# Kernel tuning notes

Hardware: AMD Instinct MI355X
Metric: run time of the kernel (lower is better)

## Reference

```python
import jax, jax.numpy as jnp
import numpy as np

B, T, N, E = 4, 8, 3000, 12000
D = 256; H = 256; HEADS = 8; DH = H // HEADS; F = 8; L = 3; HD = 64
NEG_SLOPE = 0.2


def layer_norm(x, g, b):
    m = x.mean(-1, keepdims=True)
    v = x.var(-1, keepdims=True)
    return (x - m) / jnp.sqrt(v + 1e-5) * g + b


def gat(x, edge_emb, src, dst, W, We, a_src, a_dst, a_edge):
    # x: [B,N,Din], edge_emb: [B,E,H] -> [B,N,H] via edge-conditioned graph attention
    Bc, Nc = x.shape[0], x.shape[1]
    xw = (x @ W).reshape(Bc, Nc, HEADS, DH)
    ew = (edge_emb @ We).reshape(Bc, -1, HEADS, DH)
    xs = xw[:, src]  # [B,E,HEADS,DH] gather
    xd = xw[:, dst]
    logit = (xs * a_src).sum(-1) + (xd * a_dst).sum(-1) + (ew * a_edge).sum(-1)  # [B,E,HEADS]
    logit = jnp.where(logit > 0, logit, NEG_SLOPE * logit)  # leaky_relu(0.2)

    def seg_softmax(lg):  # softmax over incoming edges per dst node
        m = jax.ops.segment_max(lg, dst, num_segments=Nc)
        e = jnp.exp(lg - m[dst])
        s = jax.ops.segment_sum(e, dst, num_segments=Nc)
        return e / (s[dst] + 1e-16)

    w = jax.vmap(seg_softmax)(logit)  # [B,E,HEADS]
    msg = (xs + ew) * w[..., None]
    out = jax.vmap(lambda m_: jax.ops.segment_sum(m_, dst, num_segments=Nc))(msg)
    return out.reshape(Bc, Nc, H)


def mlp(x, w1, b1, w2, b2):
    return jax.nn.relu(x @ w1 + b1) @ w2 + b2


def setup_inputs() -> dict:
    key = jax.random.key(0)
    ks = iter(jax.random.split(key, 64))
    rn = lambda s, sc=1.0: jax.random.normal(next(ks), s, dtype=jnp.float32) * sc
    return {
        'env_emb': rn((B, T, N, D)), 'infra_emb': rn((B, T, N, D)), 'robot_emb': rn((B, T, N, D)),
        'edge_attr': rn((B, E, F)),
        'edge_index': jax.random.randint(next(ks), (2, E), 0, N),
        'wqkv': rn((D, 3 * D), 0.05), 'bqkv': jnp.zeros((3 * D,), jnp.float32),
        'wo': rn((D, D), 0.05), 'bo': jnp.zeros((D,), jnp.float32),
        'lnf_g': jnp.ones((D,), jnp.float32), 'lnf_b': jnp.zeros((D,), jnp.float32),
        'we_emb': rn((F, H), 0.1), 'be_emb': jnp.zeros((H,), jnp.float32),
        'tg_W': rn((D, H), 0.05), 'tg_We': rn((H, H), 0.05),
        'tg_asrc': rn((HEADS, DH), 0.1), 'tg_adst': rn((HEADS, DH), 0.1), 'tg_aedge': rn((HEADS, DH), 0.1),
        'w_ih': rn((H, 4 * H), 0.05), 'w_hh': rn((H, 4 * H), 0.05), 'b_lstm': jnp.zeros((4 * H,), jnp.float32),
        'g_W': rn((L, H, H), 0.05), 'g_We': rn((L, H, H), 0.05),
        'g_asrc': rn((L, HEADS, DH), 0.1), 'g_adst': rn((L, HEADS, DH), 0.1), 'g_aedge': rn((L, HEADS, DH), 0.1),
        'g_lng': jnp.ones((L, H), jnp.float32), 'g_lnb': jnp.zeros((L, H), jnp.float32),
        'hn_w1': rn((8, H, HD), 0.05), 'hn_b1': jnp.zeros((8, HD), jnp.float32),
        'hn_w2': rn((8, HD, 1), 0.05), 'hn_b2': jnp.zeros((8, 1), jnp.float32),
        'he_w1': rn((2, 2 * H, HD), 0.05), 'he_b1': jnp.zeros((2, HD), jnp.float32),
        'he_w2': rn((2, HD, 1), 0.05), 'he_b2': jnp.zeros((2, 1), jnp.float32),
    }


def reference(env_emb, infra_emb, robot_emb, edge_attr, edge_index,
              wqkv, bqkv, wo, bo, lnf_g, lnf_b, we_emb, be_emb,
              tg_W, tg_We, tg_asrc, tg_adst, tg_aedge,
              w_ih, w_hh, b_lstm,
              g_W, g_We, g_asrc, g_adst, g_aedge, g_lng, g_lnb,
              hn_w1, hn_b1, hn_w2, hn_b2, he_w1, he_b1, he_w2, he_b2):
    # --- per-timestep 3-token cross-modal self-attention, vectorized over B,T,N ---
    tokens = jnp.stack([env_emb, infra_emb, robot_emb], axis=3)  # [B,T,N,3,D]
    qkv = tokens @ wqkv + bqkv
    q, k, v = jnp.split(qkv, 3, axis=-1)
    sh = tokens.shape[:-1] + (HEADS, DH)
    q = q.reshape(sh); k = k.reshape(sh); v = v.reshape(sh)
    att = jax.nn.softmax(jnp.einsum('btnqhd,btnkhd->btnhqk', q, k) / np.sqrt(DH).astype(np.float32), axis=-1)
    o = jnp.einsum('btnhqk,btnkhd->btnqhd', att, v).reshape(tokens.shape)
    fused_seq = layer_norm((o @ wo + bo).mean(axis=3), lnf_g, lnf_b)  # [B,T,N,D]

    edge_emb = jax.nn.relu(edge_attr @ we_emb + be_emb)  # [B,E,H]
    src = edge_index[0]; dst = edge_index[1]

    # --- TemporalGNNCell: GAT message passing feeding an LSTM cell, scanned over T ---
    def step(carry, x_t):
        h, c = carry
        m = gat(x_t, edge_emb, src, dst, tg_W, tg_We, tg_asrc, tg_adst, tg_aedge)
        gates = m @ w_ih + h @ w_hh + b_lstm
        i, f, g, oo = jnp.split(gates, 4, axis=-1)
        c = jax.nn.sigmoid(f) * c + jax.nn.sigmoid(i) * jnp.tanh(g)
        h = jax.nn.sigmoid(oo) * jnp.tanh(c)
        return (h, c), None

    z = jnp.zeros((B, N, H), fused_seq.dtype)
    (h, _), _ = jax.lax.scan(step, (z, z), jnp.moveaxis(fused_seq, 1, 0))

    # --- stacked residual GAT layers with LayerNorm ---
    for i in range(L):
        h_new = gat(h, edge_emb, src, dst, g_W[i], g_We[i], g_asrc[i], g_adst[i], g_aedge[i])
        h = layer_norm(h + h_new, g_lng[i], g_lnb[i])

    # --- prediction heads ---
    failure = jax.nn.sigmoid(mlp(h, hn_w1[0], hn_b1[0], hn_w2[0], hn_b2[0]))
    timing = jax.nn.softplus(mlp(h, hn_w1[1], hn_b1[1], hn_w2[1], hn_b2[1]))
    others = [mlp(h, hn_w1[j], hn_b1[j], hn_w2[j], hn_b2[j]) for j in range(2, 6)]  # voltage, angle, temperature, reactive
    risk = jax.nn.sigmoid(mlp(h, hn_w1[6], hn_b1[6], hn_w2[6], hn_b2[6]))
    node_out = jnp.concatenate([failure, timing] + others + [risk], axis=-1)  # [B,N,7]
    h_global = h.mean(axis=1, keepdims=True)
    freq = mlp(h_global, hn_w1[7], hn_b1[7], hn_w2[7], hn_b2[7]).reshape(B, 1)
    ef = jnp.concatenate([h[:, src], h[:, dst]], axis=-1)  # [B,E,2H]
    line = mlp(ef, he_w1[0], he_b1[0], he_w2[0], he_b2[0])
    active = mlp(ef, he_w1[1], he_b1[1], he_w2[1], he_b2[1])
    return jnp.concatenate([node_out.reshape(B, -1), line.reshape(B, -1), active.reshape(B, -1), freq], axis=1)
```

## Files before the change

kernel.cpp:

```cpp
#include <hip/hip_runtime.h>
#include <hip/hip_bf16.h>
#include <math.h>

#define DEV __device__ __forceinline__

namespace {
constexpr int B_ = 4, T_ = 8, N_ = 3000, E_ = 12000;
constexpr int OUTS_ = 45001;
}

using f32x4 = __attribute__((ext_vector_type(4))) float;
using bf16x8 = __attribute__((ext_vector_type(8))) short;

DEV float sigm_(float x) { return 1.0f / (1.0f + expf(-x)); }
DEV float softplus_(float x) { return fmaxf(x, 0.0f) + log1pf(expf(-fabsf(x))); }
DEV float wred_(float v) {
  #pragma unroll
  for (int o = 32; o > 0; o >>= 1) v += __shfl_xor(v, o, 64);
  return v;
}
DEV unsigned short f2bf(float x) {
  unsigned u = __float_as_uint(x);
  return (unsigned short)((u + 0x7FFFu + ((u >> 16) & 1u)) >> 16);
}
DEV unsigned f2bf2(float a, float b) {
  return (unsigned)f2bf(a) | ((unsigned)f2bf(b) << 16);
}
DEV float bfl(unsigned u) { return __uint_as_float(u << 16); }
DEV float bfh(unsigned u) { return __uint_as_float(u & 0xffff0000u); }

__global__ void wtb_k(const float* __restrict__ W, unsigned short* __restrict__ Wt,
                      int K, int N, int total)
{
  const int idx = blockIdx.x * blockDim.x + threadIdx.x;
  if (idx >= total) return;
  const int kn = K * N;
  const int l = idx / kn;
  const int r = idx - l * kn;
  const int k = r / N, n = r - k * N;
  Wt[(size_t)l * kn + (size_t)n * K + k] = f2bf(W[idx]);
}

__global__ void wtp_k(const float* __restrict__ W, unsigned short* __restrict__ Wt,
                      int kOff)
{
  const int idx = blockIdx.x * blockDim.x + threadIdx.x;
  if (idx >= 256 * 1024) return;
  const int k = idx >> 10;
  const int n = idx & 1023;
  const int newcol = (n & 255) * 4 + (n >> 8);
  Wt[(size_t)newcol * 512 + kOff + k] = f2bf(W[idx]);
}

__global__ void hist_k(const int* __restrict__ dst, int* __restrict__ deg)
{
  const int e = blockIdx.x * blockDim.x + threadIdx.x;
  if (e < E_) atomicAdd(&deg[dst[e]], 1);
}

__global__ __launch_bounds__(256) void scan_k(const int* __restrict__ deg,
                                              int* __restrict__ roff)
{
  __shared__ int part[256];
  const int t = threadIdx.x;
  int loc[12];
  int s = 0;
  #pragma unroll
  for (int i = 0; i < 12; ++i) {
    const int n = t * 12 + i;
    loc[i] = s;
    s += (n < N_) ? deg[n] : 0;
  }
  part[t] = s;
  __syncthreads();
  if (t == 0) {
    int run = 0;
    for (int i = 0; i < 256; ++i) { const int v = part[i]; part[i] = run; run += v; }
  }
  __syncthreads();
  const int base = part[t];
  #pragma unroll
  for (int i = 0; i < 12; ++i) {
    const int n = t * 12 + i;
    if (n < N_) roff[n] = base + loc[i];
  }
  if (t == 0) roff[N_] = E_;
}

__global__ __launch_bounds__(256) void fill_k(const int* __restrict__ dst,
                                              const int* __restrict__ roff,
                                              int* __restrict__ eord)
{
  const int n = blockIdx.x * 4 + (threadIdx.x >> 6);
  if (n >= N_) return;
  const int lane = threadIdx.x & 63;
  const unsigned long long ltm = (1ull << lane) - 1ull;
  int cnt = roff[n];
  for (int c = 0; c < E_; c += 64) {
    const int e = c + lane;
    const bool m = (e < E_) && (dst[e] == n);
    const unsigned long long mask = __ballot(m);
    if (m) eord[cnt + __popcll(mask & ltm)] = e;
    cnt += __popcll(mask);
  }
}

__global__ __launch_bounds__(256) void gemm_bfa_k(
    const unsigned short* __restrict__ A, const unsigned short* __restrict__ Wt,
    const float* __restrict__ bias, void* __restrict__ Cv,
    int M, int N, int K, int lda, int flags)
{
  __shared__ unsigned short Al[128 * 40];
  __shared__ unsigned short Bl[64 * 40];
  const int tid = threadIdx.x;
  const int bm = blockIdx.y * 128;
  const int bn = blockIdx.x * 64;
  const int lane = tid & 63;
  const int wv = tid >> 6;
  const int wm = (wv >> 1) * 64;
  const int wn = (wv & 1) * 32;
  const int s_row = tid >> 1;
  const int s_cb = (tid & 1) * 16;
  const int grow = bm + s_row;
  const unsigned short* Arow = (grow < M) ? A + (size_t)grow * lda : nullptr;
  const int b_col = tid >> 2;
  const int b_ks = (tid & 3) * 8;
  const unsigned short* Wrow = Wt + (size_t)(bn + b_col) * K + b_ks;

  f32x4 acc[4][2] = {};
  const int l15 = lane & 15;
  const int lk = (lane >> 4) * 8;

  for (int k0 = 0; k0 < K; k0 += 32) {
    uint4 a0, a1;
    if (Arow) {
      a0 = *(const uint4*)(Arow + k0 + s_cb);
      a1 = *(const uint4*)(Arow + k0 + s_cb + 8);
    } else {
      a0 = make_uint4(0, 0, 0, 0);
      a1 = a0;
    }
    *(uint4*)&Al[s_row * 40 + s_cb] = a0;
    *(uint4*)&Al[s_row * 40 + s_cb + 8] = a1;
    *(uint4*)&Bl[b_col * 40 + b_ks] = *(const uint4*)(Wrow + k0);
    __syncthreads();
    bf16x8 af[4], bfr[2];
    #pragma unroll
    for (int m = 0; m < 4; ++m)
      af[m] = *(const bf16x8*)&Al[(wm + m * 16 + l15) * 40 + lk];
    #pragma unroll
    for (int n = 0; n < 2; ++n)
      bfr[n] = *(const bf16x8*)&Bl[(wn + n * 16 + l15) * 40 + lk];
    #pragma unroll
    for (int m = 0; m < 4; ++m)
      #pragma unroll
      for (int n = 0; n < 2; ++n)
        acc[m][n] = __builtin_amdgcn_mfma_f32_16x16x32_bf16(af[m], bfr[n], acc[m][n], 0, 0, 0);
    __syncthreads();
  }
  float* Cf = (float*)Cv;
  unsigned short* Cb = (unsigned short*)Cv;
  const int r4 = (lane >> 4) * 4;
  #pragma unroll
  for (int m = 0; m < 4; ++m) {
    #pragma unroll
    for (int n = 0; n < 2; ++n) {
      const int col = bn + wn + n * 16 + l15;
      const float bv = bias ? bias[col] : 0.f;
      #pragma unroll
      for (int r = 0; r < 4; ++r) {
        const int row = bm + wm + m * 16 + r4 + r;
        if (row >= M) continue;
        float v = acc[m][n][r] + bv;
        const size_t ci = (size_t)row * N + col;
        if (flags & 1) v += Cf[ci];
        if (flags & 2) v = fmaxf(v, 0.f);
        if (flags & 4) Cb[ci] = f2bf(v);
        else Cf[ci] = v;
      }
    }
  }
}

__global__ __launch_bounds__(256) void gemm_qkv_k(
    const float* __restrict__ env, const float* __restrict__ infra,
    const float* __restrict__ robot, const unsigned short* __restrict__ Wt,
    const float* __restrict__ bias, unsigned short* __restrict__ Cb,
    int M, int nodeBase)
{
  __shared__ unsigned short Al[128 * 40];
  __shared__ unsigned short Bl[64 * 40];
  const int tid = threadIdx.x;
  const int bm = blockIdx.y * 128;
  const int bn = blockIdx.x * 64;
  const int lane = tid & 63;
  const int wv = tid >> 6;
  const int wm = (wv >> 1) * 64;
  const int wn = (wv & 1) * 32;
  const int s_row = tid >> 1;
  const int s_cb = (tid & 1) * 16;
  const int grow = bm + s_row;
  const float* Arow = nullptr;
  if (grow < M) {
    const int slot = grow % 3;
    const int node = nodeBase + grow / 3;
    const float* srcp = (slot == 0 ? env : (slot == 1 ? infra : robot));
    Arow = srcp + (size_t)node * 256;
  }
  const int b_col = tid >> 2;
  const int b_ks = (tid & 3) * 8;
  const unsigned short* Wrow = Wt + (size_t)(bn + b_col) * 256 + b_ks;

  f32x4 acc[4][2] = {};
  const int l15 = lane & 15;
  const int lk = (lane >> 4) * 8;

  for (int k0 = 0; k0 < 256; k0 += 32) {
    unsigned abuf[8];
    if (Arow) {
      const float* p = Arow + k0 + s_cb;
      #pragma unroll
      for (int i = 0; i < 4; ++i) {
        const float4 v = *(const float4*)(p + i * 4);
        abuf[i * 2 + 0] = f2bf2(v.x, v.y);
        abuf[i * 2 + 1] = f2bf2(v.z, v.w);
      }
    } else {
      #pragma unroll
      for (int i = 0; i < 8; ++i) abuf[i] = 0;
    }
    *(uint4*)&Al[s_row * 40 + s_cb] = *(uint4*)&abuf[0];
    *(uint4*)&Al[s_row * 40 + s_cb + 8] = *(uint4*)&abuf[4];
    *(uint4*)&Bl[b_col * 40 + b_ks] = *(const uint4*)(Wrow + k0);
    __syncthreads();
    bf16x8 af[4], bfr[2];
    #pragma unroll
    for (int m = 0; m < 4; ++m)
      af[m] = *(const bf16x8*)&Al[(wm + m * 16 + l15) * 40 + lk];
    #pragma unroll
    for (int n = 0; n < 2; ++n)
      bfr[n] = *(const bf16x8*)&Bl[(wn + n * 16 + l15) * 40 + lk];
    #pragma unroll
    for (int m = 0; m < 4; ++m)
      #pragma unroll
      for (int n = 0; n < 2; ++n)
        acc[m][n] = __builtin_amdgcn_mfma_f32_16x16x32_bf16(af[m], bfr[n], acc[m][n], 0, 0, 0);
    __syncthreads();
  }
  const int r4 = (lane >> 4) * 4;
  #pragma unroll
  for (int m = 0; m < 4; ++m) {
    #pragma unroll
    for (int n = 0; n < 2; ++n) {
      const int col = bn + wn + n * 16 + l15;
      const float bv = bias[col];
      #pragma unroll
      for (int r = 0; r < 4; ++r) {
        const int row = bm + wm + m * 16 + r4 + r;
        if (row >= M) continue;
        Cb[(size_t)row * 768 + col] = f2bf(acc[m][n][r] + bv);
      }
    }
  }
}

__global__ __launch_bounds__(256) void gemm_lstm_k(
    const unsigned short* __restrict__ gatall, const unsigned short* __restrict__ hbIn,
    const unsigned short* __restrict__ Wt, const float* __restrict__ b_lstm,
    float* __restrict__ h, float* __restrict__ c, unsigned short* __restrict__ hbOut,
    int t)
{
  __shared__ float Gl[128][65];
  unsigned short* Al = (unsigned short*)&Gl[0][0];
  unsigned short* Bl = Al + 128 * 40;
  const int tid = threadIdx.x;
  const int bm = blockIdx.y * 128;
  const int bn = blockIdx.x * 64;
  const int lane = tid & 63;
  const int wv = tid >> 6;
  const int wm = (wv >> 1) * 64;
  const int wn = (wv & 1) * 32;
  const int s_row = tid >> 1;
  const int s_cb = (tid & 1) * 16;
  const int grow = bm + s_row;
  const unsigned short* Arow1 = nullptr;
  const unsigned short* Arow2 = nullptr;
  if (grow < 12000) {
    const int phys = (grow / N_) * (T_ * N_) + t * N_ + (grow % N_);
    Arow1 = gatall + (size_t)phys * 256;
    Arow2 = hbIn + (size_t)grow * 256;
  }
  const int b_col = tid >> 2;
  const int b_ks = (tid & 3) * 8;
  const unsigned short* Wrow = Wt + (size_t)(bn + b_col) * 512 + b_ks;

  f32x4 acc[4][2] = {};
  const int l15 = lane & 15;
  const int lk = (lane >> 4) * 8;

  for (int k0 = 0; k0 < 512; k0 += 32) {
    uint4 a0, a1;
    if (Arow1) {
      const unsigned short* p = (k0 < 256) ? (Arow1 + k0 + s_cb)
                                           : (Arow2 + (k0 - 256) + s_cb);
      a0 = *(const uint4*)p;
      a1 = *(const uint4*)(p + 8);
    } else {
      a0 = make_uint4(0, 0, 0, 0);
      a1 = a0;
    }
    *(uint4*)&Al[s_row * 40 + s_cb] = a0;
    *(uint4*)&Al[s_row * 40 + s_cb + 8] = a1;
    *(uint4*)&Bl[b_col * 40 + b_ks] = *(const uint4*)(Wrow + k0);
    __syncthreads();
    bf16x8 af[4], bfr[2];
    #pragma unroll
    for (int m = 0; m < 4; ++m)
      af[m] = *(const bf16x8*)&Al[(wm + m * 16 + l15) * 40 + lk];
    #pragma unroll
    for (int n = 0; n < 2; ++n)
      bfr[n] = *(const bf16x8*)&Bl[(wn + n * 16 + l15) * 40 + lk];
    #pragma unroll
    for (int m = 0; m < 4; ++m)
      #pragma unroll
      for (int n = 0; n < 2; ++n)
        acc[m][n] = __builtin_amdgcn_mfma_f32_16x16x32_bf16(af[m], bfr[n], acc[m][n], 0, 0, 0);
    __syncthreads();
  }
  const int r4 = (lane >> 4) * 4;
  #pragma unroll
  for (int m = 0; m < 4; ++m)
    #pragma unroll
    for (int n = 0; n < 2; ++n) {
      const int col = wn + n * 16 + l15;
      #pragma unroll
      for (int r = 0; r < 4; ++r)
        Gl[wm + m * 16 + r4 + r][col] = acc[m][n][r];
    }
  __syncthreads();
  const int fl = lane & 7;
  const int rg = lane >> 3;
  const int dg = ((bn + wn) >> 2) + fl;
  const float bi = b_lstm[dg];
  const float bff = b_lstm[256 + dg];
  const float bg = b_lstm[512 + dg];
  const float bo = b_lstm[768 + dg];
  const int colb = wn + fl * 4;
  #pragma unroll
  for (int i = 0; i < 8; ++i) {
    const int rl = rg + i * 8;
    const int row = bm + wm + rl;
    if (row >= 12000) continue;
    const float g0 = Gl[wm + rl][colb + 0] + bi;
    const float g1 = Gl[wm + rl][colb + 1] + bff;
    const float g2 = Gl[wm + rl][colb + 2] + bg;
    const float g3 = Gl[wm + rl][colb + 3] + bo;
    const size_t idx = (size_t)row * 256 + dg;
    const float cn = sigm_(g1) * c[idx] + sigm_(g0) * tanhf(g2);
    c[idx] = cn;
    const float hn = sigm_(g3) * tanhf(cn);
    h[idx] = hn;
    hbOut[idx] = f2bf(hn);
  }
}

__global__ __launch_bounds__(256) void gemm_k(
    const float* __restrict__ A, const float* __restrict__ W,
    const float* __restrict__ bias, void* __restrict__ Cv,
    int M, int N, int K, int lda, int flags)
{
  __shared__ float As[16][68];
  __shared__ float Ws[16][64];
  const int tid = threadIdx.x;
  const int bm = blockIdx.y * 64;
  const int bn = blockIdx.x * 64;
  const int tx = tid & 15;
  const int ty = tid >> 4;
  const int ar = tid >> 2;
  const int ac = (tid & 3) << 2;
  const int wr = tid >> 4;
  const int wc = (tid & 15) << 2;
  const int grow = bm + ar;
  const float* Arow = (grow < M) ? A + (size_t)grow * lda : nullptr;
  float acc[4][4] = {};
  for (int k0 = 0; k0 < K; k0 += 16) {
    float4 av = make_float4(0.f, 0.f, 0.f, 0.f);
    if (Arow) {
      av.x = (k0 + ac + 0 < K) ? Arow[k0 + ac + 0] : 0.f;
      av.y = (k0 + ac + 1 < K) ? Arow[k0 + ac + 1] : 0.f;
      av.z = (k0 + ac + 2 < K) ? Arow[k0 + ac + 2] : 0.f;
      av.w = (k0 + ac + 3 < K) ? Arow[k0 + ac + 3] : 0.f;
    }
    As[ac + 0][ar] = av.x;
    As[ac + 1][ar] = av.y;
    As[ac + 2][ar] = av.z;
    As[ac + 3][ar] = av.w;
    float4 wv = make_float4(0.f, 0.f, 0.f, 0.f);
    if (k0 + wr < K) {
      const int gc = bn + wc;
      const float* wp = W + (size_t)(k0 + wr) * N + gc;
      wv.x = (gc + 0 < N) ? wp[0] : 0.f;
      wv.y = (gc + 1 < N) ? wp[1] : 0.f;
      wv.z = (gc + 2 < N) ? wp[2] : 0.f;
      wv.w = (gc + 3 < N) ? wp[3] : 0.f;
    }
    *(float4*)&Ws[wr][wc] = wv;
    __syncthreads();
    #pragma unroll
    for (int kk = 0; kk < 16; ++kk) {
      const float4 a = *(const float4*)&As[kk][ty << 2];
      const float4 b = *(const float4*)&Ws[kk][tx << 2];
      acc[0][0] += a.x * b.x; acc[0][1] += a.x * b.y; acc[0][2] += a.x * b.z; acc[0][3] += a.x * b.w;
      acc[1][0] += a.y * b.x; acc[1][1] += a.y * b.y; acc[1][2] += a.y * b.z; acc[1][3] += a.y * b.w;
      acc[2][0] += a.z * b.x; acc[2][1] += a.z * b.y; acc[2][2] += a.z * b.z; acc[2][3] += a.z * b.w;
      acc[3][0] += a.w * b.x; acc[3][1] += a.w * b.y; acc[3][2] += a.w * b.z; acc[3][3] += a.w * b.w;
    }
    __syncthreads();
  }
  float* Cf = (float*)Cv;
  unsigned short* Cb = (unsigned short*)Cv;
  #pragma unroll
  for (int i = 0; i < 4; ++i) {
    const int row = bm + (ty << 2) + i;
    if (row >= M) continue;
    #pragma unroll
    for (int j = 0; j < 4; ++j) {
      const int col = bn + (tx << 2) + j;
      if (col >= N) continue;
      float v = acc[i][j];
      if (bias) v += bias[col];
      if (flags & 2) v = fmaxf(v, 0.f);
      const size_t ci = (size_t)row * N + col;
      if (flags & 4) Cb[ci] = f2bf(v);
      else Cf[ci] = v;
    }
  }
}

__global__ __launch_bounds__(256) void attn_avg_k(
    const unsigned short* __restrict__ qkv,
    unsigned short* __restrict__ obar, int nodes)
{
  const int node = blockIdx.x * 4 + (threadIdx.x >> 6);
  if (node >= nodes) return;
  const int lane = threadIdx.x & 63;
  const unsigned short* base = qkv + (size_t)node * 2304 + lane * 4;
  float qv[3][4], kv[3][4], vv[3][4];
  #pragma unroll
  for (int s = 0; s < 3; ++s) {
    const uint2 uq = *(const uint2*)(base + s * 768);
    const uint2 uk = *(const uint2*)(base + s * 768 + 256);
    const uint2 uv = *(const uint2*)(base + s * 768 + 512);
    qv[s][0] = bfl(uq.x); qv[s][1] = bfh(uq.x); qv[s][2] = bfl(uq.y); qv[s][3] = bfh(uq.y);
    kv[s][0] = bfl(uk.x); kv[s][1] = bfh(uk.x); kv[s][2] = bfl(uk.y); kv[s][3] = bfh(uk.y);
    vv[s][0] = bfl(uv.x); vv[s][1] = bfh(uv.x); vv[s][2] = bfl(uv.y); vv[s][3] = bfh(uv.y);
  }
  float att[3][3];
  #pragma unroll
  for (int s = 0; s < 3; ++s) {
    #pragma unroll
    for (int t = 0; t < 3; ++t) {
      float d = qv[s][0] * kv[t][0] + qv[s][1] * kv[t][1]
              + qv[s][2] * kv[t][2] + qv[s][3] * kv[t][3];
      d += __shfl_xor(d, 1, 64);
      d += __shfl_xor(d, 2, 64);
      d += __shfl_xor(d, 4, 64);
      att[s][t] = d * 0.17677669529663687f;
    }
  }
  float cs[3] = {0.f, 0.f, 0.f};
  #pragma unroll
  for (int s = 0; s < 3; ++s) {
    const float m = fmaxf(att[s][0], fmaxf(att[s][1], att[s][2]));
    const float e0 = expf(att[s][0] - m);
    const float e1 = expf(att[s][1] - m);
    const float e2 = expf(att[s][2] - m);
    const float inv = (1.f / 3.f) / (e0 + e1 + e2);
    cs[0] += e0 * inv; cs[1] += e1 * inv; cs[2] += e2 * inv;
  }
  float o0 = cs[0] * vv[0][0] + cs[1] * vv[1][0] + cs[2] * vv[2][0];
  float o1 = cs[0] * vv[0][1] + cs[1] * vv[1][1] + cs[2] * vv[2][1];
  float o2 = cs[0] * vv[0][2] + cs[1] * vv[1][2] + cs[2] * vv[2][2];
  float o3 = cs[0] * vv[0][3] + cs[1] * vv[1][3] + cs[2] * vv[2][3];
  uint2 ob;
  ob.x = f2bf2(o0, o1);
  ob.y = f2bf2(o2, o3);
  *(uint2*)(obar + (size_t)node * 256 + lane * 4) = ob;
}

__global__ __launch_bounds__(64) void ln_k(
    const float* __restrict__ in, const float* __restrict__ g,
    const float* __restrict__ bta, unsigned short* __restrict__ outp)
{
  const int row = blockIdx.x;
  const int d0 = threadIdx.x << 2;
  const float4 a = *(const float4*)(in + (size_t)row * 256 + d0);
  float x[4] = { a.x, a.y, a.z, a.w };
  float s = x[0] + x[1] + x[2] + x[3];
  s = wred_(s);
  const float mean = s * (1.f / 256.f);
  float vs = 0.f;
  #pragma unroll
  for (int i = 0; i < 4; ++i) { const float dd = x[i] - mean; vs += dd * dd; }
  vs = wred_(vs);
  const float inv = 1.0f / sqrtf(vs * (1.f / 256.f) + 1e-5f);
  const float4 gv = *(const float4*)(g + d0);
  const float4 bv = *(const float4*)(bta + d0);
  uint2 o;
  o.x = f2bf2((x[0] - mean) * inv * gv.x + bv.x, (x[1] - mean) * inv * gv.y + bv.y);
  o.y = f2bf2((x[2] - mean) * inv * gv.z + bv.z, (x[3] - mean) * inv * gv.w + bv.w);
  *(uint2*)(outp + (size_t)row * 256 + d0) = o;
}

__global__ void alphas_k(const unsigned short* __restrict__ xw, const float* __restrict__ as,
                         const float* __restrict__ ad, float* __restrict__ sal,
                         float* __restrict__ dal, int rows)
{
  const int idx = blockIdx.x * blockDim.x + threadIdx.x;
  if (idx >= rows * 8) return;
  const int row = idx >> 3, h = idx & 7;
  const unsigned short* x = xw + (size_t)row * 256 + h * 32;
  const float* a1 = as + h * 32;
  const float* a2 = ad + h * 32;
  float s = 0.f, d = 0.f;
  #pragma unroll
  for (int i = 0; i < 4; ++i) {
    const uint4 ux = *(const uint4*)(x + i * 8);
    const unsigned* p = &ux.x;
    #pragma unroll
    for (int j = 0; j < 4; ++j) {
      const float lo = bfl(p[j]), hi = bfh(p[j]);
      s += lo * a1[i * 8 + 2 * j] + hi * a1[i * 8 + 2 * j + 1];
      d += lo * a2[i * 8 + 2 * j] + hi * a2[i * 8 + 2 * j + 1];
    }
  }
  sal[idx] = s; dal[idx] = d;
}

__global__ void elog4_k(const unsigned short* __restrict__ ew,
                        const float* __restrict__ tg_ae, const float* __restrict__ g_ae,
                        float* __restrict__ el)
{
  const int idx = blockIdx.x * blockDim.x + threadIdx.x;
  if (idx >= 4 * 48000 * 8) return;
  const int l = idx / (48000 * 8);
  const int r = idx - l * (48000 * 8);
  const int row = r >> 3, h = r & 7;
  const unsigned short* x = ew + (size_t)row * 1024 + l * 256 + h * 32;
  const float* a1 = (l == 0 ? tg_ae : g_ae + (l - 1) * 256) + h * 32;
  float s = 0.f;
  #pragma unroll
  for (int i = 0; i < 4; ++i) {
    const uint4 ux = *(const uint4*)(x + i * 8);
    const unsigned* p = &ux.x;
    #pragma unroll
    for (int j = 0; j < 4; ++j) {
      s += bfl(p[j]) * a1[i * 8 + 2 * j] + bfh(p[j]) * a1[i * 8 + 2 * j + 1];
    }
  }
  el[l * 384000 + r] = s;
}

template<int OUTBF>
__global__ __launch_bounds__(256) void gat_k(
    const unsigned short* __restrict__ xw, const unsigned short* __restrict__ ew,
    const float* __restrict__ sal, const float* __restrict__ dal,
    const float* __restrict__ el, const int* __restrict__ roff,
    const int* __restrict__ eord, const int* __restrict__ srcArr,
    void* __restrict__ outp, int nwaves, int tshift, int ewStride, int ewOff)
{
  const int wid = blockIdx.x * 4 + (threadIdx.x >> 6);
  if (wid >= nwaves) return;
  const int beta = wid / N_;
  const int n = wid - beta * N_;
  const int b = beta >> tshift;
  const int lane = threadIdx.x & 63;
  const int h = lane >> 3;
  const int d0 = lane << 2;
  const float dal_h = dal[(size_t)wid * 8 + h];
  const int p0 = roff[n], p1 = roff[n + 1];
  float m = -1e30f, s = 0.f;
  float4 acc = make_float4(0.f, 0.f, 0.f, 0.f);
  for (int p = p0; p < p1; ++p) {
    const int e = eord[p];
    const int sc = srcArr[e];
    float lg = sal[((size_t)beta * N_ + sc) * 8 + h] + dal_h + el[((size_t)b * E_ + e) * 8 + h];
    lg = lg > 0.f ? lg : 0.2f * lg;
    const float mn = fmaxf(m, lg);
    const float scale = expf(m - mn);
    const float w = expf(lg - mn);
    s = s * scale + w;
    const uint2 ux = *(const uint2*)(xw + ((size_t)beta * N_ + sc) * 256 + d0);
    const uint2 ue = *(const uint2*)(ew + ((size_t)(b * E_ + e)) * ewStride + ewOff + d0);
    acc.x = acc.x * scale + w * (bfl(ux.x) + bfl(ue.x));
    acc.y = acc.y * scale + w * (bfh(ux.x) + bfh(ue.x));
    acc.z = acc.z * scale + w * (bfl(ux.y) + bfl(ue.y));
    acc.w = acc.w * scale + w * (bfh(ux.y) + bfh(ue.y));
    m = mn;
  }
  const float inv = 1.0f / (s + 1e-16f);
  if (OUTBF) {
    uint2 o;
    o.x = f2bf2(acc.x * inv, acc.y * inv);
    o.y = f2bf2(acc.z * inv, acc.w * inv);
    *(uint2*)((unsigned short*)outp + (size_t)wid * 256 + d0) = o;
  } else {
    *(float4*)((float*)outp + (size_t)wid * 256 + d0) =
        make_float4(acc.x * inv, acc.y * inv, acc.z * inv, acc.w * inv);
  }
}

__global__ __launch_bounds__(64) void resln_k(float* __restrict__ h,
                                              const float* __restrict__ add,
                                              const float* __restrict__ g,
                                              const float* __restrict__ bta,
                                              unsigned short* __restrict__ hb)
{
  const int row = blockIdx.x;
  const int d0 = threadIdx.x << 2;
  float* hp = h + (size_t)row * 256;
  const float4 hv = *(const float4*)(hp + d0);
  const float4 av = *(const float4*)(add + (size_t)row * 256 + d0);
  float x[4] = { hv.x + av.x, hv.y + av.y, hv.z + av.z, hv.w + av.w };
  float s = x[0] + x[1] + x[2] + x[3];
  s = wred_(s);
  const float mean = s * (1.f / 256.f);
  float vs = 0.f;
  #pragma unroll
  for (int i = 0; i < 4; ++i) { const float dd = x[i] - mean; vs += dd * dd; }
  vs = wred_(vs);
  const float inv = 1.0f / sqrtf(vs * (1.f / 256.f) + 1e-5f);
  const float4 gv = *(const float4*)(g + d0);
  const float4 bv = *(const float4*)(bta + d0);
  float o0 = (x[0] - mean) * inv * gv.x + bv.x;
  float o1 = (x[1] - mean) * inv * gv.y + bv.y;
  float o2 = (x[2] - mean) * inv * gv.z + bv.z;
  float o3 = (x[3] - mean) * inv * gv.w + bv.w;
  *(float4*)(hp + d0) = make_float4(o0, o1, o2, o3);
  uint2 ob;
  ob.x = f2bf2(o0, o1);
  ob.y = f2bf2(o2, o3);
  *(uint2*)(hb + (size_t)row * 256 + d0) = ob;
}

__global__ void nh2_k(const float* __restrict__ hidden, const float* __restrict__ w2,
                      const float* __restrict__ b2, float* __restrict__ outp)
{
  const int idx = blockIdx.x * blockDim.x + threadIdx.x;
  if (idx >= B_ * N_ * 7) return;
  const int row = idx / 7, j = idx % 7;
  const float* hp = hidden + (size_t)row * 448 + j * 64;
  const float* wp = w2 + j * 64;
  float a = 0.f;
  #pragma unroll
  for (int u = 0; u < 64; ++u) a += hp[u] * wp[u];
  a += b2[j];
  if (j == 0 || j == 6) a = sigm_(a);
  else if (j == 1) a = softplus_(a);
  const int b = row / N_, n = row % N_;
  outp[(size_t)b * OUTS_ + n * 7 + j] = a;
}

__global__ __launch_bounds__(256) void hglob1_k(const float* __restrict__ h,
                                                float* __restrict__ hgp)
{
  const int b = blockIdx.x;
  const int seg = blockIdx.y;
  const int d = threadIdx.x;
  float s = 0.f;
  const int n0 = seg * 120;
  for (int n = n0; n < n0 + 120; ++n)
    s += h[((size_t)(b * N_ + n)) * 256 + d];
  hgp[((size_t)(b * 25 + seg)) * 256 + d] = s;
}

__global__ __launch_bounds__(256) void hglob2_k(const float* __restrict__ hgp,
                                                float* __restrict__ hg)
{
  const int b = blockIdx.x;
  const int d = threadIdx.x;
  float s = 0.f;
  for (int i = 0; i < 25; ++i) s += hgp[((size_t)(b * 25 + i)) * 256 + d];
  hg[b * 256 + d] = s * (1.f / (float)N_);
}

__global__ __launch_bounds__(64) void freq_k(const float* __restrict__ hg,
                                             const float* __restrict__ w1, const float* __restrict__ b1,
                                             const float* __restrict__ w2, const float* __restrict__ b2,
                                             float* __restrict__ outp)
{
  const int b = blockIdx.x;
  const int u = threadIdx.x;
  float a = b1[u];
  for (int k = 0; k < 256; ++k) a += hg[b * 256 + k] * w1[k * 64 + u];
  a = fmaxf(a, 0.f) * w2[u];
  a = wred_(a);
  if (u == 0) outp[(size_t)b * OUTS_ + 45000] = a + b2[0];
}

__global__ void ef_k(const unsigned short* __restrict__ hb, const int* __restrict__ src,
                     const int* __restrict__ dst, unsigned short* __restrict__ ef)
{
  const int idx = blockIdx.x * blockDim.x + threadIdx.x;
  if (idx >= B_ * E_ * 64) return;
  const int q = idx & 63;
  const int row = idx >> 6;
  const int b = row / E_, e = row % E_;
  const int d = q << 3;
  const unsigned short* p = (d < 256)
      ? hb + ((size_t)(b * N_ + src[e])) * 256 + d
      : hb + ((size_t)(b * N_ + dst[e])) * 256 + (d - 256);
  *(uint4*)(ef + (size_t)row * 512 + d) = *(const uint4*)p;
}

__global__ void eh2_k(const float* __restrict__ hidden, const float* __restrict__ w2,
                      const float* __restrict__ b2, float* __restrict__ outp)
{
  const int idx = blockIdx.x * blockDim.x + threadIdx.x;
  if (idx >= 2 * B_ * E_) return;
  const int jj = idx / (B_ * E_);
  const int r = idx - jj * (B_ * E_);
  const int b = r / E_, e = r % E_;
  const float* hp = hidden + (size_t)r * 128 + jj * 64;
  const float* wp = w2 + jj * 64;
  float a = 0.f;
  #pragma unroll
  for (int u = 0; u < 64; ++u) a += hp[u] * wp[u];
  a += b2[jj];
  outp[(size_t)b * OUTS_ + 21000 + jj * 12000 + e] = a;
}

extern "C" void kernel_launch(void* const* d_in, const int* in_sizes, int n_in,
                              void* d_out, int out_size, void* d_ws, size_t ws_size,
                              hipStream_t stream)
{
  const float* env      = (const float*)d_in[0];
  const float* infra    = (const float*)d_in[1];
  const float* robot    = (const float*)d_in[2];
  const float* edgeattr = (const float*)d_in[3];
  const int*   eidx     = (const int*)d_in[4];
  const float* wqkv     = (const float*)d_in[5];
  const float* bqkv     = (const float*)d_in[6];
  const float* wo       = (const float*)d_in[7];
  const float* bo       = (const float*)d_in[8];
  const float* lnf_g    = (const float*)d_in[9];
  const float* lnf_b    = (const float*)d_in[10];
  const float* we_emb   = (const float*)d_in[11];
  const float* be_emb   = (const float*)d_in[12];
  const float* tg_W     = (const float*)d_in[13];
  const float* tg_We    = (const float*)d_in[14];
  const float* tg_asrc  = (const float*)d_in[15];
  const float* tg_adst  = (const float*)d_in[16];
  const float* tg_aedge = (const float*)d_in[17];
  const float* w_ih     = (const float*)d_in[18];
  const float* w_hh     = (const float*)d_in[19];
  const float* b_lstm   = (const float*)d_in[20];
  const float* g_W      = (const float*)d_in[21];
  const float* g_We     = (const float*)d_in[22];
  const float* g_asrc   = (const float*)d_in[23];
  const float* g_adst   = (const float*)d_in[24];
  const float* g_aedge  = (const float*)d_in[25];
  const float* g_lng    = (const float*)d_in[26];
  const float* g_lnb    = (const float*)d_in[27];
  const float* hn_w1    = (const float*)d_in[28];
  const float* hn_b1    = (const float*)d_in[29];
  const float* hn_w2    = (const float*)d_in[30];
  const float* hn_b2    = (const float*)d_in[31];
  const float* he_w1    = (const float*)d_in[32];
  const float* he_b1    = (const float*)d_in[33];
  const float* he_w2    = (const float*)d_in[34];
  const float* he_b2    = (const float*)d_in[35];

  const int* src = eidx;
  const int* dst = eidx + E_;
  float* outp = (float*)d_out;
  float* ws = (float*)d_ws;

  unsigned short* wtb0 = (unsigned short*)ws;
  unsigned short* wt_qkv  = wtb0;
  unsigned short* wt_wo   = wtb0 + 196608;
  unsigned short* wt_tgW  = wtb0 + 262144;
  unsigned short* wt_tgWe = wtb0 + 327680;
  unsigned short* wt_gWe  = wtb0 + 393216;
  unsigned short* wt_lstm = wtb0 + 589824;
  unsigned short* wt_gW   = wtb0 + 1114112;
  unsigned short* wt_hn   = wtb0 + 1310720;
  unsigned short* wt_he   = wtb0 + 1425408;

  const size_t D0 = 1600000;
  unsigned short* qkvb  = (unsigned short*)(ws + D0);
  float* tmpA = ws + D0 + 13824000;
  unsigned short* obarb = (unsigned short*)(ws + D0 + 38400000);
  unsigned short* fseqb = (unsigned short*)(ws + D0 + 50688000);
  unsigned short* xwallb  = (unsigned short*)(ws + D0);
  unsigned short* gatallb = (unsigned short*)(ws + D0 + 12288000);
  unsigned short* eembb   = (unsigned short*)(ws + D0 + 24576000);
  float* h  = ws + D0 + 30720000;
  float* c  = ws + D0 + 33792000;
  unsigned short* hb0 = (unsigned short*)(ws + D0 + 36864000);
  unsigned short* hb1 = (unsigned short*)(ws + D0 + 38400000);
  unsigned short* ewall = (unsigned short*)(ws + D0 + 62976000);
  float* elogall = ws + D0 + 87552000;
  float* sal     = ws + D0 + 89088000;
  float* dal     = ws + D0 + 89856000;
  int* ideg  = (int*)(ws + D0 + 90624000);
  int* iroff = ideg + 3008;
  int* ieord = iroff + 3008;
  float* hg  = ws + D0 + 90650000;
  float* hgp = ws + D0 + 90652048;
  unsigned short* xw_sb = (unsigned short*)(ws + D0 + 40000000);
  float* gat_s = ws + D0 + 41600000;
  float* hidn = ws + D0;
  unsigned short* efb = (unsigned short*)(ws + D0 + 5376000);
  float* hide = ws + D0 + 17664000;

  auto mgemm = [&](const unsigned short* A, const unsigned short* Wt, const float* bias,
                   void* C, int M, int N, int K, int lda, int flags) {
    dim3 grid(N / 64, (M + 127) / 128);
    gemm_bfa_k<<<grid, dim3(256), 0, stream>>>(A, Wt, bias, C, M, N, K, lda, flags);
  };
  auto cvtb = [&](const float* W, unsigned short* Wt, int K, int N, int L) {
    const int total = K * N * L;
    wtb_k<<<(total + 255) / 256, 256, 0, stream>>>(W, Wt, K, N, total);
  };

  cvtb(wqkv, wt_qkv, 256, 768, 1);
  cvtb(wo, wt_wo, 256, 256, 1);
  cvtb(tg_W, wt_tgW, 256, 256, 1);
  cvtb(tg_We, wt_tgWe, 256, 256, 1);
  cvtb(g_We, wt_gWe, 256, 256, 3);
  wtp_k<<<1024, 256, 0, stream>>>(w_ih, wt_lstm, 0);
  wtp_k<<<1024, 256, 0, stream>>>(w_hh, wt_lstm, 256);
  cvtb(g_W, wt_gW, 256, 256, 3);
  cvtb(hn_w1, wt_hn, 256, 64, 7);
  cvtb(he_w1, wt_he, 512, 64, 2);

  hipMemsetAsync(ideg, 0, 3000 * sizeof(int), stream);
  hist_k<<<(E_ + 255) / 256, 256, 0, stream>>>(dst, ideg);
  scan_k<<<1, 256, 0, stream>>>(ideg, iroff);
  fill_k<<<750, 256, 0, stream>>>(dst, iroff, ieord);

  for (int chunk = 0; chunk < 8; ++chunk) {
    dim3 grid(768 / 64, (36000 + 127) / 128);
    gemm_qkv_k<<<grid, dim3(256), 0, stream>>>(env, infra, robot, wt_qkv, bqkv,
                                               qkvb, 36000, chunk * 12000);
    attn_avg_k<<<3000, 256, 0, stream>>>(qkvb, obarb + (size_t)chunk * 12000 * 256, 12000);
  }
  mgemm(obarb, wt_wo, bo, tmpA, 96000, 256, 256, 256, 0);
  ln_k<<<96000, 64, 0, stream>>>(tmpA, lnf_g, lnf_b, fseqb);

  {
    dim3 grid(4, 750);
    gemm_k<<<grid, dim3(256), 0, stream>>>(edgeattr, we_emb, be_emb, eembb,
                                           48000, 256, 8, 8, 2 | 4);
  }
  mgemm(eembb, wt_tgWe, nullptr, ewall, 48000, 1024, 256, 256, 4);
  elog4_k<<<6000, 256, 0, stream>>>(ewall, tg_aedge, g_aedge, elogall);

  mgemm(fseqb, wt_tgW, nullptr, xwallb, 96000, 256, 256, 256, 4);
  alphas_k<<<3000, 256, 0, stream>>>(xwallb, tg_asrc, tg_adst, sal, dal, 96000);
  gat_k<1><<<24000, 256, 0, stream>>>(xwallb, ewall, sal, dal, elogall, iroff, ieord,
                                      src, gatallb, 96000, 3, 1024, 0);

  hipMemsetAsync(c, 0, 12288000, stream);
  hipMemsetAsync(hb0, 0, 6144000, stream);
  unsigned short* hbq[2] = { hb0, hb1 };
  for (int t = 0; t < T_; ++t) {
    dim3 grid(16, 94);
    gemm_lstm_k<<<grid, dim3(256), 0, stream>>>(gatallb, hbq[t & 1], wt_lstm, b_lstm,
                                                h, c, hbq[(t + 1) & 1], t);
  }
  unsigned short* hbf = hbq[0];

  for (int l = 0; l < 3; ++l) {
    mgemm(hbf, wt_gW + (size_t)l * 65536, nullptr, xw_sb, 12000, 256, 256, 256, 4);
    alphas_k<<<375, 256, 0, stream>>>(xw_sb, g_asrc + l * 256, g_adst + l * 256, sal, dal, 12000);
    gat_k<0><<<3000, 256, 0, stream>>>(xw_sb, ewall, sal, dal, elogall + 384000 * (l + 1),
                                       iroff, ieord, src, gat_s, 12000, 0,
                                       1024, 256 * (l + 1));
    resln_k<<<12000, 64, 0, stream>>>(h, gat_s, g_lng + l * 256, g_lnb + l * 256, hbf);
  }

  mgemm(hbf, wt_hn, hn_b1, hidn, 12000, 448, 256, 256, 2);
  nh2_k<<<(84000 + 255) / 256, 256, 0, stream>>>(hidn, hn_w2, hn_b2, outp);

  hglob1_k<<<dim3(4, 25), 256, 0, stream>>>(h, hgp);
  hglob2_k<<<4, 256, 0, stream>>>(hgp, hg);
  freq_k<<<4, 64, 0, stream>>>(hg, hn_w1 + 7 * 16384, hn_b1 + 7 * 64,
                               hn_w2 + 7 * 64, hn_b2 + 7, outp);

  ef_k<<<12000, 256, 0, stream>>>(hbf, src, dst, efb);
  mgemm(efb, wt_he, he_b1, hide, 48000, 128, 512, 512, 2);
  eh2_k<<<(96000 + 255) / 256, 256, 0, stream>>>(hide, he_w2, he_b2, outp);
}
```

Baseline: 1.692 ms.

## Fuse QKV projection GEMM with 3-token attention averaging in one kernel

Replaces the chunked QKV GEMM plus separate attention-average kernel with a single kernel. Each block computes all 768 QKV columns for 16 nodes (48 rows), stages Q/K and then V in shared memory, and writes only the averaged output. This removes the large bf16 QKV intermediate's global round trip and 16 launches. The Wo projection output is also stored as bf16 instead of fp32 before LayerNorm, halving that traffic at some precision cost. The new kernel uses about 64KB of LDS and 144 accumulator registers, which may lower occupancy.

```diff
diff --git a/kernel.cpp b/kernel.cpp
--- a/kernel.cpp
+++ b/kernel.cpp
@@ -26,6 +26,7 @@
 DEV unsigned f2bf2(float a, float b) {
   return (unsigned)f2bf(a) | ((unsigned)f2bf(b) << 16);
 }
+DEV float bfs(unsigned short u) { return __uint_as_float((unsigned)u << 16); }
 DEV float bfl(unsigned u) { return __uint_as_float(u << 16); }
 DEV float bfh(unsigned u) { return __uint_as_float(u & 0xffff0000u); }
 
@@ -182,85 +183,162 @@
   }
 }
 
-__global__ __launch_bounds__(256) void gemm_qkv_k(
+__global__ __launch_bounds__(256) void qkv_attn_k(
     const float* __restrict__ env, const float* __restrict__ infra,
     const float* __restrict__ robot, const unsigned short* __restrict__ Wt,
-    const float* __restrict__ bias, unsigned short* __restrict__ Cb,
-    int M, int nodeBase)
-{
-  __shared__ unsigned short Al[128 * 40];
-  __shared__ unsigned short Bl[64 * 40];
+    const float* __restrict__ bias, unsigned short* __restrict__ obar)
+{
+  __shared__ unsigned short U[32640];
+  unsigned short* Al = U;
+  unsigned short* Bl = U + 1920;
+  unsigned short* P  = U;
+  float* csL = (float*)(U + 25088);
+
   const int tid = threadIdx.x;
-  const int bm = blockIdx.y * 128;
-  const int bn = blockIdx.x * 64;
   const int lane = tid & 63;
   const int wv = tid >> 6;
-  const int wm = (wv >> 1) * 64;
-  const int wn = (wv & 1) * 32;
-  const int s_row = tid >> 1;
-  const int s_cb = (tid & 1) * 16;
-  const int grow = bm + s_row;
-  const float* Arow = nullptr;
-  if (grow < M) {
-    const int slot = grow % 3;
-    const int node = nodeBase + grow / 3;
-    const float* srcp = (slot == 0 ? env : (slot == 1 ? infra : robot));
-    Arow = srcp + (size_t)node * 256;
-  }
-  const int b_col = tid >> 2;
-  const int b_ks = (tid & 3) * 8;
-  const unsigned short* Wrow = Wt + (size_t)(bn + b_col) * 256 + b_ks;
-
-  f32x4 acc[4][2] = {};
   const int l15 = lane & 15;
   const int lk = (lane >> 4) * 8;
+  const int r4 = (lane >> 4) * 4;
+  const int nodeBase = blockIdx.x * 16;
+
+  const float* Asrc = nullptr;
+  int a_ks = 0, a_row = 0;
+  if (tid < 192) {
+    a_row = tid >> 2;
+    a_ks = (tid & 3) * 8;
+    const int grow = blockIdx.x * 48 + a_row;
+    const int node = grow / 3, slot = grow % 3;
+    const float* sp = (slot == 0 ? env : (slot == 1 ? infra : robot));
+    Asrc = sp + (size_t)node * 256 + a_ks;
+  }
+
+  f32x4 acc[3][12] = {};
 
   for (int k0 = 0; k0 < 256; k0 += 32) {
-    unsigned abuf[8];
-    if (Arow) {
-      const float* p = Arow + k0 + s_cb;
+    if (Asrc) {
+      const float4 v0 = *(const float4*)(Asrc + k0);
+      const float4 v1 = *(const float4*)(Asrc + k0 + 4);
+      uint4 o;
+      o.x = f2bf2(v0.x, v0.y); o.y = f2bf2(v0.z, v0.w);
+      o.z = f2bf2(v1.x, v1.y); o.w = f2bf2(v1.z, v1.w);
+      *(uint4*)&Al[a_row * 40 + a_ks] = o;
+    }
+    #pragma unroll
+    for (int i = 0; i < 12; ++i) {
+      const int task = tid + i * 256;
+      const int col = task >> 2;
+      const int ks = (task & 3) * 8;
+      *(uint4*)&Bl[col * 40 + ks] = *(const uint4*)(Wt + (size_t)col * 256 + k0 + ks);
+    }
+    __syncthreads();
+    bf16x8 af[3];
+    #pragma unroll
+    for (int m = 0; m < 3; ++m)
+      af[m] = *(const bf16x8*)&Al[(m * 16 + l15) * 40 + lk];
+    #pragma unroll
+    for (int n = 0; n < 12; ++n) {
+      const bf16x8 bfr = *(const bf16x8*)&Bl[(wv * 192 + n * 16 + l15) * 40 + lk];
       #pragma unroll
-      for (int i = 0; i < 4; ++i) {
-        const float4 v = *(const float4*)(p + i * 4);
-        abuf[i * 2 + 0] = f2bf2(v.x, v.y);
-        abuf[i * 2 + 1] = f2bf2(v.z, v.w);
+      for (int m = 0; m < 3; ++m)
+        acc[m][n] = __builtin_amdgcn_mfma_f32_16x16x32_bf16(af[m], bfr, acc[m][n], 0, 0, 0);
+    }
+    __syncthreads();
+  }
+
+  #pragma unroll
+  for (int n = 0; n < 12; ++n) {
+    const int pcol = wv * 192 + n * 16 + l15;
+    if (pcol < 512) {
+      const float bv = bias[pcol];
+      #pragma unroll
+      for (int m = 0; m < 3; ++m)
+        #pragma unroll
+        for (int r = 0; r < 4; ++r)
+          P[(m * 16 + r4 + r) * 520 + pcol] = f2bf(acc[m][n][r] + bv);
+    }
+  }
+  __syncthreads();
+
+  const int h = lane >> 3;
+  const int j = (lane & 7) * 4;
+  #pragma unroll
+  for (int q = 0; q < 4; ++q) {
+    const int nb = wv * 4 + q;
+    float qv[3][4], kv[3][4];
+    #pragma unroll
+    for (int s = 0; s < 3; ++s) {
+      const int row = nb * 3 + s;
+      const uint2 uq = *(const uint2*)&P[row * 520 + h * 32 + j];
+      const uint2 uk = *(const uint2*)&P[row * 520 + 256 + h * 32 + j];
+      qv[s][0] = bfl(uq.x); qv[s][1] = bfh(uq.x); qv[s][2] = bfl(uq.y); qv[s][3] = bfh(uq.y);
+      kv[s][0] = bfl(uk.x); kv[s][1] = bfh(uk.x); kv[s][2] = bfl(uk.y); kv[s][3] = bfh(uk.y);
+    }
+    float att[3][3];
+    #pragma unroll
+    for (int s = 0; s < 3; ++s)
+      #pragma unroll
+      for (int t = 0; t < 3; ++t) {
+        float d = qv[s][0] * kv[t][0] + qv[s][1] * kv[t][1]
+                + qv[s][2] * kv[t][2] + qv[s][3] * kv[t][3];
+        d += __shfl_xor(d, 1, 64);
+        d += __shfl_xor(d, 2, 64);
+        d += __shfl_xor(d, 4, 64);
+        att[s][t] = d * 0.17677669529663687f;
       }
-    } else {
+    float cs[3] = {0.f, 0.f, 0.f};
+    #pragma unroll
+    for (int s = 0; s < 3; ++s) {
+      const float m = fmaxf(att[s][0], fmaxf(att[s][1], att[s][2]));
+      const float e0 = expf(att[s][0] - m);
+      const float e1 = expf(att[s][1] - m);
+      const float e2 = expf(att[s][2] - m);
+      const float inv = (1.f / 3.f) / (e0 + e1 + e2);
+      cs[0] += e0 * inv; cs[1] += e1 * inv; cs[2] += e2 * inv;
+    }
+    if ((lane & 7) == 0) {
+      csL[nb * 24 + h * 3 + 0] = cs[0];
+      csL[nb * 24 + h * 3 + 1] = cs[1];
+      csL[nb * 24 + h * 3 + 2] = cs[2];
+    }
+  }
+  __syncthreads();
+
+  #pragma unroll
+  for (int n = 0; n < 12; ++n) {
+    const int pcol = wv * 192 + n * 16 + l15;
+    if (pcol >= 512) {
+      const float bv = bias[pcol];
+      const int vc = pcol - 512;
       #pragma unroll
-      for (int i = 0; i < 8; ++i) abuf[i] = 0;
-    }
-    *(uint4*)&Al[s_row * 40 + s_cb] = *(uint4*)&abuf[0];
-    *(uint4*)&Al[s_row * 40 + s_cb + 8] = *(uint4*)&abuf[4];
-    *(uint4*)&Bl[b_col * 40 + b_ks] = *(const uint4*)(Wrow + k0);
-    __syncthreads();
-    bf16x8 af[4], bfr[2];
-    #pragma unroll
-    for (int m = 0; m < 4; ++m)
-      af[m] = *(const bf16x8*)&Al[(wm + m * 16 + l15) * 40 + lk];
-    #pragma unroll
-    for (int n = 0; n < 2; ++n)
-      bfr[n] = *(const bf16x8*)&Bl[(wn + n * 16 + l15) * 40 + lk];
-    #pragma unroll
-    for (int m = 0; m < 4; ++m)
-      #pragma unroll
-      for (int n = 0; n < 2; ++n)
-        acc[m][n] = __builtin_amdgcn_mfma_f32_16x16x32_bf16(af[m], bfr[n], acc[m][n], 0, 0, 0);
-    __syncthreads();
-  }
-  const int r4 = (lane >> 4) * 4;
-  #pragma unroll
-  for (int m = 0; m < 4; ++m) {
-    #pragma unroll
-    for (int n = 0; n < 2; ++n) {
-      const int col = bn + wn + n * 16 + l15;
-      const float bv = bias[col];
-      #pragma unroll
-      for (int r = 0; r < 4; ++r) {
-        const int row = bm + wm + m * 16 + r4 + r;
-        if (row >= M) continue;
-        Cb[(size_t)row * 768 + col] = f2bf(acc[m][n][r] + bv);
-      }
-    }
+      for (int m = 0; m < 3; ++m)
+        #pragma unroll
+        for (int r = 0; r < 4; ++r)
+          P[(m * 16 + r4 + r) * 272 + vc] = f2bf(acc[m][n][r] + bv);
+    }
+  }
+  __syncthreads();
+
+  #pragma unroll
+  for (int q = 0; q < 4; ++q) {
+    const int nb = wv * 4 + q;
+    const float c0 = csL[nb * 24 + h * 3 + 0];
+    const float c1 = csL[nb * 24 + h * 3 + 1];
+    const float c2 = csL[nb * 24 + h * 3 + 2];
+    float o[4] = {0.f, 0.f, 0.f, 0.f};
+    const float cc[3] = {c0, c1, c2};
+    #pragma unroll
+    for (int s = 0; s < 3; ++s) {
+      const uint2 uv = *(const uint2*)&P[(nb * 3 + s) * 272 + h * 32 + j];
+      o[0] += cc[s] * bfl(uv.x);
+      o[1] += cc[s] * bfh(uv.x);
+      o[2] += cc[s] * bfl(uv.y);
+      o[3] += cc[s] * bfh(uv.y);
+    }
+    uint2 ob;
+    ob.x = f2bf2(o[0], o[1]);
+    ob.y = f2bf2(o[2], o[3]);
+    *(uint2*)(obar + (size_t)(nodeBase + nb) * 256 + lane * 4) = ob;
   }
 }
 
@@ -437,65 +515,14 @@
   }
 }
 
-__global__ __launch_bounds__(256) void attn_avg_k(
-    const unsigned short* __restrict__ qkv,
-    unsigned short* __restrict__ obar, int nodes)
-{
-  const int node = blockIdx.x * 4 + (threadIdx.x >> 6);
-  if (node >= nodes) return;
-  const int lane = threadIdx.x & 63;
-  const unsigned short* base = qkv + (size_t)node * 2304 + lane * 4;
-  float qv[3][4], kv[3][4], vv[3][4];
-  #pragma unroll
-  for (int s = 0; s < 3; ++s) {
-    const uint2 uq = *(const uint2*)(base + s * 768);
-    const uint2 uk = *(const uint2*)(base + s * 768 + 256);
-    const uint2 uv = *(const uint2*)(base + s * 768 + 512);
-    qv[s][0] = bfl(uq.x); qv[s][1] = bfh(uq.x); qv[s][2] = bfl(uq.y); qv[s][3] = bfh(uq.y);
-    kv[s][0] = bfl(uk.x); kv[s][1] = bfh(uk.x); kv[s][2] = bfl(uk.y); kv[s][3] = bfh(uk.y);
-    vv[s][0] = bfl(uv.x); vv[s][1] = bfh(uv.x); vv[s][2] = bfl(uv.y); vv[s][3] = bfh(uv.y);
-  }
-  float att[3][3];
-  #pragma unroll
-  for (int s = 0; s < 3; ++s) {
-    #pragma unroll
-    for (int t = 0; t < 3; ++t) {
-      float d = qv[s][0] * kv[t][0] + qv[s][1] * kv[t][1]
-              + qv[s][2] * kv[t][2] + qv[s][3] * kv[t][3];
-      d += __shfl_xor(d, 1, 64);
-      d += __shfl_xor(d, 2, 64);
-      d += __shfl_xor(d, 4, 64);
-      att[s][t] = d * 0.17677669529663687f;
-    }
-  }
-  float cs[3] = {0.f, 0.f, 0.f};
-  #pragma unroll
-  for (int s = 0; s < 3; ++s) {
-    const float m = fmaxf(att[s][0], fmaxf(att[s][1], att[s][2]));
-    const float e0 = expf(att[s][0] - m);
-    const float e1 = expf(att[s][1] - m);
-    const float e2 = expf(att[s][2] - m);
-    const float inv = (1.f / 3.f) / (e0 + e1 + e2);
-    cs[0] += e0 * inv; cs[1] += e1 * inv; cs[2] += e2 * inv;
-  }
-  float o0 = cs[0] * vv[0][0] + cs[1] * vv[1][0] + cs[2] * vv[2][0];
-  float o1 = cs[0] * vv[0][1] + cs[1] * vv[1][1] + cs[2] * vv[2][1];
-  float o2 = cs[0] * vv[0][2] + cs[1] * vv[1][2] + cs[2] * vv[2][2];
-  float o3 = cs[0] * vv[0][3] + cs[1] * vv[1][3] + cs[2] * vv[2][3];
-  uint2 ob;
-  ob.x = f2bf2(o0, o1);
-  ob.y = f2bf2(o2, o3);
-  *(uint2*)(obar + (size_t)node * 256 + lane * 4) = ob;
-}
-
 __global__ __launch_bounds__(64) void ln_k(
-    const float* __restrict__ in, const float* __restrict__ g,
+    const unsigned short* __restrict__ in, const float* __restrict__ g,
     const float* __restrict__ bta, unsigned short* __restrict__ outp)
 {
   const int row = blockIdx.x;
   const int d0 = threadIdx.x << 2;
-  const float4 a = *(const float4*)(in + (size_t)row * 256 + d0);
-  float x[4] = { a.x, a.y, a.z, a.w };
+  const uint2 a = *(const uint2*)(in + (size_t)row * 256 + d0);
+  float x[4] = { bfl(a.x), bfh(a.x), bfl(a.y), bfh(a.y) };
   float s = x[0] + x[1] + x[2] + x[3];
   s = wred_(s);
   const float mean = s * (1.f / 256.f);
@@ -788,9 +815,8 @@
   unsigned short* wt_he   = wtb0 + 1425408;
 
   const size_t D0 = 1600000;
-  unsigned short* qkvb  = (unsigned short*)(ws + D0);
-  float* tmpA = ws + D0 + 13824000;
-  unsigned short* obarb = (unsigned short*)(ws + D0 + 38400000);
+  unsigned short* obarb = (unsigned short*)(ws + D0);
+  unsigned short* tmpAb = (unsigned short*)(ws + D0 + 12288000);
   unsigned short* fseqb = (unsigned short*)(ws + D0 + 50688000);
   unsigned short* xwallb  = (unsigned short*)(ws + D0);
   unsigned short* gatallb = (unsigned short*)(ws + D0 + 12288000);
@@ -840,14 +866,9 @@
   scan_k<<<1, 256, 0, stream>>>(ideg, iroff);
   fill_k<<<750, 256, 0, stream>>>(dst, iroff, ieord);
 
-  for (int chunk = 0; chunk < 8; ++chunk) {
-    dim3 grid(768 / 64, (36000 + 127) / 128);
-    gemm_qkv_k<<<grid, dim3(256), 0, stream>>>(env, infra, robot, wt_qkv, bqkv,
-                                               qkvb, 36000, chunk * 12000);
-    attn_avg_k<<<3000, 256, 0, stream>>>(qkvb, obarb + (size_t)chunk * 12000 * 256, 12000);
-  }
-  mgemm(obarb, wt_wo, bo, tmpA, 96000, 256, 256, 256, 0);
-  ln_k<<<96000, 64, 0, stream>>>(tmpA, lnf_g, lnf_b, fseqb);
+  qkv_attn_k<<<6000, 256, 0, stream>>>(env, infra, robot, wt_qkv, bqkv, obarb);
+  mgemm(obarb, wt_wo, bo, tmpAb, 96000, 256, 256, 256, 4);
+  ln_k<<<96000, 64, 0, stream>>>(tmpAb, lnf_g, lnf_b, fseqb);
 
   {
     dim3 grid(4, 750);
```

Result: slower. 1.771 ms (+4.6%).
